# Kernel tuning notes

Measured on AMD Instinct MI355X. Metric: run time of the kernel, lower is better.

## Reference

```python
import jax, jax.numpy as jnp
import numpy as np

M = 64; N_SC = 32; SPS = 8; LENCP = 16; NUMOFDM = 256 // N_SC
BETA = 0.5; SPAN = 16; LENRRC = SPAN * SPS + 1  # 129
FC = 25e6; FS = 10e6 * SPS
CLIP = 1.2; SNR = 10.0; THRES = 8.0
LEN_T = NUMOFDM * (M + LENCP)              # 640
NUMSAMPLES = LEN_T * SPS + LENRRC * 2      # 5378
L1 = LEN_T * SPS + LENRRC - 1              # 5248 (post pulse-shaping length)


def make_rrc():
    # standard root-raised-cosine, unit energy
    t = np.arange(-SPAN * SPS // 2, SPAN * SPS // 2 + 1) / SPS
    h = np.zeros_like(t)
    eps = 1e-9
    t0 = np.abs(t) < eps
    ts = np.abs(np.abs(t) - 1.0 / (4 * BETA)) < eps
    reg = ~(t0 | ts)
    tr = t[reg]
    h[reg] = (np.sin(np.pi * tr * (1 - BETA)) + 4 * BETA * tr * np.cos(np.pi * tr * (1 + BETA))) / (
        np.pi * tr * (1 - (4 * BETA * tr) ** 2))
    h[t0] = 1 + BETA * (4 / np.pi - 1)
    h[ts] = (BETA / np.sqrt(2)) * ((1 + 2 / np.pi) * np.sin(np.pi / (4 * BETA)) +
                                   (1 - 2 / np.pi) * np.cos(np.pi / (4 * BETA)))
    h = h / np.sqrt(np.sum(h ** 2))
    return h.astype(np.float32)


def _conv_full(u, k):
    # torch F.conv1d(x, k.flip(), padding=K-1) == full convolution with k
    K = k.shape[0]
    return jax.lax.conv_general_dilated(
        u[:, None, :], k[::-1][None, None, :], (1,), [(K - 1, K - 1)],
        dimension_numbers=('NCH', 'OIH', 'NCH'))[:, 0, :]


def _pulse_filter(c, rrc):
    return _conv_full(c.real, rrc) + 1j * _conv_full(c.imag, rrc)


def _power_norm(z):
    m = jnp.mean(z, axis=1, keepdims=True)
    s = jnp.std(z, axis=1, ddof=1, keepdims=True)  # torch.std is unbiased
    return (z - m) / (s + 1e-8)


def _forward(x, W_enc, b_enc, W_dec, b_dec, rrc, awgn, startloc):
    B = x.shape[0]
    # --- encoder (linear proxy for ResNetTx) -> 512 reals ---
    z = x.reshape(B, -1) @ W_enc + b_enc
    z = _power_norm(z)
    c = z.reshape(B, 256, 2)
    c = (c[..., 0] + 1j * c[..., 1]).reshape(B, NUMOFDM, N_SC)  # complex64
    # --- DFT precoding ---
    c = jnp.fft.fftshift(jnp.fft.fft(c, axis=-1, norm='ortho'), axes=-1)
    # --- subcarrier mapping (contiguous block, mapping==1) ---
    loc = jnp.arange(startloc, startloc + N_SC)
    data_f = jnp.zeros((B, NUMOFDM, M), jnp.complex64).at[:, :, loc].set(c)
    data_t = jnp.fft.ifft(data_f, axis=-1, norm='ortho')
    data_t = jnp.concatenate([data_t[:, :, -LENCP:], data_t], axis=-1)  # CP
    data_t = data_t.reshape(B, LEN_T)
    # --- zero-stuffed upsampling + RRC pulse shaping ---
    over = jnp.zeros((B, LEN_T * SPS), jnp.complex64).at[:, ::SPS].set(data_t)
    xc = _pulse_filter(over, rrc)  # (B, L1)
    # --- carrier mixing ---
    n = jnp.arange(NUMSAMPLES, dtype=jnp.float32)
    cos_c = jnp.sqrt(2.0) * jnp.cos(2 * jnp.pi * FC * n / FS)
    sin_c = jnp.sqrt(2.0) * jnp.sin(2 * jnp.pi * FC * n / FS)
    data_x = xc.real * cos_c[:L1] - xc.imag * sin_c[:L1]
    # --- clipping ---
    thr = CLIP * jnp.sqrt(jnp.mean(jnp.square(data_x), axis=1, keepdims=True))
    over_amp = jax.nn.relu(jnp.abs(data_x) - thr)
    data_x = (1.0 - over_amp / (jnp.abs(data_x) + 1e-8)) * data_x
    # --- PAPR ---
    tstart = (LENRRC + 1) // 2
    p = jnp.square(data_x[:, tstart:tstart + LEN_T * SPS])
    PAPRdB = 10.0 * jnp.log10(jnp.max(p, axis=1) / jnp.mean(p, axis=1))
    PAPRloss = jnp.mean(jax.nn.relu(PAPRdB - THRES))
    # --- AWGN channel (no fading) ---
    data_r = data_x + awgn
    # --- downconversion + matched filter ---
    rc = data_r * cos_c[:L1] - 1j * (data_r * sin_c[:L1])
    filt = _pulse_filter(rc, rrc)  # (B, L1 + LENRRC - 1) = (B, 5376)
    y = filt[:, LENRRC - 1:filt.shape[1] - LENRRC:SPS]  # (B, LEN_T)
    y = y.reshape(B, NUMOFDM, M + LENCP)[:, :, LENCP:]
    y = jnp.fft.fft(y, axis=-1, norm='ortho')[:, :, loc]
    y = jnp.fft.ifft(jnp.fft.fftshift(y, axes=-1), axis=-1, norm='ortho')
    y = y.reshape(B, NUMOFDM * N_SC)
    y = jnp.stack([y.real, y.imag], axis=-1).reshape(B, 8, 8, 8)
    # --- decoder (linear proxy for ResNetRx) ---
    out = (y.reshape(B, 512) @ W_dec + b_dec).reshape(B, 3, 32, 32)
    return out, PAPRdB, PAPRloss


def setup_inputs() -> dict:
    key = jax.random.key(0)
    ks = jax.random.split(key, 4)
    B = 1024
    x = jax.random.normal(ks[0], (B, 3, 32, 32), jnp.float32)
    W_enc = jax.random.normal(ks[1], (3072, 512), jnp.float32) * 0.02
    b_enc = jnp.zeros((512,), jnp.float32)
    W_dec = jax.random.normal(ks[2], (512, 3072), jnp.float32) * 0.05
    b_dec = jnp.zeros((3072,), jnp.float32)
    rrc = jnp.asarray(make_rrc())
    noise_std = 10.0 ** (-SNR / 20.0)
    awgn = jax.random.normal(ks[3], (B, L1), jnp.float32) * noise_std
    return {"x": x, "W_enc": W_enc, "b_enc": b_enc, "W_dec": W_dec,
            "b_dec": b_dec, "rrc": rrc, "awgn": awgn, "startloc": 7}


def reference(x, W_enc, b_enc, W_dec, b_dec, rrc, awgn, startloc):
    return _forward(x, W_enc, b_enc, W_dec, b_dec, rrc, awgn, startloc)
```

## Files before the change

kernel.cpp:

```cpp
#include <hip/hip_runtime.h>
#include <hip/hip_bf16.h>
#include <math.h>

#define L1_     5248
#define LENRRC_ 129
#define TSTART_ 65
#define NWIN_   5120
#define SWZ(m) ((m) + ((m) >> 3))

typedef __attribute__((ext_vector_type(8))) short s16x8;
typedef __attribute__((ext_vector_type(4))) float f32x4;

__device__ inline ushort bf16_rne(float x) {
    unsigned xb = __float_as_uint(x);
    return (ushort)((xb + 0x7fffu + ((xb >> 16) & 1u)) >> 16);
}

__device__ inline float wave_sum(float v) {
    #pragma unroll
    for (int m = 32; m > 0; m >>= 1) v += __shfl_xor(v, m, 64);
    return v;
}
__device__ inline float wave_max(float v) {
    #pragma unroll
    for (int m = 32; m > 0; m >>= 1) v = fmaxf(v, __shfl_xor(v, m, 64));
    return v;
}

__device__ inline void gl_lds16(const void* g, void* l) {
    __builtin_amdgcn_global_load_lds(
        (const __attribute__((address_space(1))) unsigned int*)g,
        (__attribute__((address_space(3))) unsigned int*)l, 16, 0, 0);
}

__global__ __launch_bounds__(256) void pack_k(const float* __restrict__ x,
        const float* __restrict__ W1, const float* __restrict__ W2,
        const float* __restrict__ benc,
        ushort* __restrict__ xb, ushort* __restrict__ w1t, ushort* __restrict__ w2t,
        float* __restrict__ z)
{
    __shared__ ushort tile[64][70];
    const int blk = blockIdx.x, tid = threadIdx.x;
    if (blk < 3072) {
        int i = blk * 256 + tid;
        float4 v = ((const float4*)x)[i];
        ushort4 h;
        h.x = bf16_rne(v.x); h.y = bf16_rne(v.y);
        h.z = bf16_rne(v.z); h.w = bf16_rne(v.w);
        ((ushort4*)xb)[i] = h;
    } else if (blk < 3840) {
        const float* W; ushort* T; int K, N, n0, k0;
        if (blk < 3456) {
            int idx = blk - 3072;
            W = W1; T = w1t; K = 3072; N = 512;
            n0 = (idx & 7) * 64; k0 = (idx >> 3) * 64;
        } else {
            int idx = blk - 3456;
            W = W2; T = w2t; K = 512; N = 3072;
            n0 = (idx % 48) * 64; k0 = (idx / 48) * 64;
        }
        const int cr = tid >> 4, cc = (tid & 15) * 4;
        #pragma unroll
        for (int i = 0; i < 4; ++i) {
            int kk = i * 16 + cr;
            float4 v = *(const float4*)&W[(size_t)(k0 + kk) * N + n0 + cc];
            tile[kk][cc]     = bf16_rne(v.x);
            tile[kk][cc + 1] = bf16_rne(v.y);
            tile[kk][cc + 2] = bf16_rne(v.z);
            tile[kk][cc + 3] = bf16_rne(v.w);
        }
        __syncthreads();
        #pragma unroll
        for (int i = 0; i < 4; ++i) {
            int nn = i * 16 + cr;
            ushort4 h;
            h.x = tile[cc][nn]; h.y = tile[cc + 1][nn];
            h.z = tile[cc + 2][nn]; h.w = tile[cc + 3][nn];
            *(ushort4*)&T[(size_t)(n0 + nn) * K + k0 + cc] = h;
        }
    } else {
        int i = (blk - 3840) * 256 + tid;
        z[i] = benc[i & 511];
    }
}

__global__ __launch_bounds__(256) void gemm1_k(const ushort* __restrict__ Ab,
        const ushort* __restrict__ Bb, float* __restrict__ C, int M, int N, int K,
        int partial)
{
    __shared__ __attribute__((aligned(16))) ushort Asl[64 * 64];
    __shared__ __attribute__((aligned(16))) ushort Bsl[128 * 64];
    const int tid = threadIdx.x;
    const int lane = tid & 63, wave = tid >> 6;
    const int wm = (wave >> 1) * 32, wn = (wave & 1) * 64;
    const int m0 = blockIdx.y * 64, n0 = blockIdx.x * 128;
    const int kch = K / 8, kbeg = blockIdx.z * kch, kend = kbeg + kch;
    const int fm = lane & 15, q = lane >> 4;
    f32x4 acc[2][4] = {};

    int arow[2], akb[2], brow[4], bkb[4];
    #pragma unroll
    for (int j = 0; j < 2; ++j) {
        int c = ((wave * 2 + j) << 6) + lane;
        arow[j] = c >> 3; akb[j] = (c & 7) ^ (arow[j] & 7);
    }
    #pragma unroll
    for (int j = 0; j < 4; ++j) {
        int c = ((wave * 4 + j) << 6) + lane;
        brow[j] = c >> 3; bkb[j] = (c & 7) ^ (brow[j] & 7);
    }

    for (int kt = kbeg; kt < kend; kt += 64) {
        #pragma unroll
        for (int j = 0; j < 2; ++j)
            gl_lds16(&Ab[(size_t)(m0 + arow[j]) * K + kt + akb[j] * 8],
                     &Asl[(wave * 2 + j) << 9]);
        #pragma unroll
        for (int j = 0; j < 4; ++j)
            gl_lds16(&Bb[(size_t)(n0 + brow[j]) * K + kt + bkb[j] * 8],
                     &Bsl[(wave * 4 + j) << 9]);
        __syncthreads();
        #pragma unroll
        for (int ks = 0; ks < 2; ++ks) {
            s16x8 a[2], b[4];
            #pragma unroll
            for (int mf = 0; mf < 2; ++mf) {
                int r = wm + mf * 16 + fm;
                a[mf] = *(const s16x8*)&Asl[(r << 6) + ((((ks << 2) + q) ^ (r & 7)) << 3)];
            }
            #pragma unroll
            for (int nf = 0; nf < 4; ++nf) {
                int r = wn + nf * 16 + fm;
                b[nf] = *(const s16x8*)&Bsl[(r << 6) + ((((ks << 2) + q) ^ (r & 7)) << 3)];
            }
            #pragma unroll
            for (int mf = 0; mf < 2; ++mf)
                #pragma unroll
                for (int nf = 0; nf < 4; ++nf)
                    acc[mf][nf] = __builtin_amdgcn_mfma_f32_16x16x32_bf16(a[mf], b[nf], acc[mf][nf], 0, 0, 0);
        }
        __syncthreads();
    }

    if (partial) {
        float* Cs = C + (size_t)blockIdx.z * ((size_t)M * N);
        #pragma unroll
        for (int mf = 0; mf < 2; ++mf)
            #pragma unroll
            for (int nf = 0; nf < 4; ++nf)
                #pragma unroll
                for (int r = 0; r < 4; ++r) {
                    int m = m0 + wm + mf * 16 + q * 4 + r;
                    int n = n0 + wn + nf * 16 + fm;
                    Cs[(size_t)m * N + n] = acc[mf][nf][r];
                }
    } else {
        #pragma unroll
        for (int mf = 0; mf < 2; ++mf)
            #pragma unroll
            for (int nf = 0; nf < 4; ++nf)
                #pragma unroll
                for (int r = 0; r < 4; ++r) {
                    int m = m0 + wm + mf * 16 + q * 4 + r;
                    int n = n0 + wn + nf * 16 + fm;
                    atomicAdd(&C[(size_t)m * N + n], acc[mf][nf][r]);
                }
    }
}

__global__ __launch_bounds__(256) void gemm2_k(const ushort* __restrict__ Ab,
        const ushort* __restrict__ Bb, const float* __restrict__ bias,
        const float* __restrict__ papr, float* __restrict__ C,
        float* __restrict__ out_loss, int M, int N, int K)
{
    __shared__ __attribute__((aligned(16))) ushort Asl[64 * 64];
    __shared__ __attribute__((aligned(16))) ushort Bsl[64 * 64];
    __shared__ float red[4];
    const int tid = threadIdx.x;
    const int lane = tid & 63, wave = tid >> 6;
    const int wm = (wave >> 1) * 32, wn = (wave & 1) * 32;
    const int m0 = blockIdx.y * 64, n0 = blockIdx.x * 64;
    const int fm = lane & 15, q = lane >> 4;
    f32x4 acc[2][2] = {};

    int srow[2], skb[2];
    #pragma unroll
    for (int j = 0; j < 2; ++j) {
        int c = ((wave * 2 + j) << 6) + lane;
        srow[j] = c >> 3; skb[j] = (c & 7) ^ (srow[j] & 7);
    }

    for (int kt = 0; kt < K; kt += 64) {
        #pragma unroll
        for (int j = 0; j < 2; ++j) {
            gl_lds16(&Ab[(size_t)(m0 + srow[j]) * K + kt + skb[j] * 8],
                     &Asl[(wave * 2 + j) << 9]);
            gl_lds16(&Bb[(size_t)(n0 + srow[j]) * K + kt + skb[j] * 8],
                     &Bsl[(wave * 2 + j) << 9]);
        }
        __syncthreads();
        #pragma unroll
        for (int ks = 0; ks < 2; ++ks) {
            s16x8 a[2], b[2];
            #pragma unroll
            for (int mf = 0; mf < 2; ++mf) {
                int r = wm + mf * 16 + fm;
                a[mf] = *(const s16x8*)&Asl[(r << 6) + ((((ks << 2) + q) ^ (r & 7)) << 3)];
            }
            #pragma unroll
            for (int nf = 0; nf < 2; ++nf) {
                int r = wn + nf * 16 + fm;
                b[nf] = *(const s16x8*)&Bsl[(r << 6) + ((((ks << 2) + q) ^ (r & 7)) << 3)];
            }
            #pragma unroll
            for (int mf = 0; mf < 2; ++mf)
                #pragma unroll
                for (int nf = 0; nf < 2; ++nf)
                    acc[mf][nf] = __builtin_amdgcn_mfma_f32_16x16x32_bf16(a[mf], b[nf], acc[mf][nf], 0, 0, 0);
        }
        __syncthreads();
    }

    #pragma unroll
    for (int mf = 0; mf < 2; ++mf)
        #pragma unroll
        for (int nf = 0; nf < 2; ++nf)
            #pragma unroll
            for (int r = 0; r < 4; ++r) {
                int m = m0 + wm + mf * 16 + q * 4 + r;
                int n = n0 + wn + nf * 16 + fm;
                C[(size_t)m * N + n] = acc[mf][nf][r] + bias[n];
            }

    if (blockIdx.x == 0 && blockIdx.y == 0) {
        float s = 0.f;
        for (int i = tid; i < 1024; i += 256) { float v = papr[i] - 8.f; s += v > 0.f ? v : 0.f; }
        s = wave_sum(s);
        if (lane == 0) red[wave] = s;
        __syncthreads();
        if (tid == 0) *out_loss = (red[0] + red[1] + red[2] + red[3]) * (1.f / 1024.f);
    }
}

__global__ __launch_bounds__(512, 8) void mega_k(const float* __restrict__ z,
        const float* __restrict__ benc,
        const float* __restrict__ rrc, const float* __restrict__ awgn,
        const int* __restrict__ slocp, ushort* __restrict__ y5b,
        float* __restrict__ papr, float* __restrict__ out_papr, int nsp)
{
    __shared__ float  zl[512];
    __shared__ float2 frfi[8][32];
    __shared__ float2 trti[672];
    __shared__ float  hl[132];
    __shared__ float  csl[16], ssl[16];
    __shared__ float2 cs64[64];
    __shared__ float2 gcs[130];
    __shared__ float  dxr[SWZ(L1_ - 1) + 1];
    __shared__ float2 wrli[512];
    __shared__ float  red[8], red2[8];

    const int b = blockIdx.x, tid = threadIdx.x;
    const int lane = tid & 63, wv = tid >> 6;
    const int sloc = *slocp;

    if (tid < 64) {
        float ang = 0.09817477042468103f * (float)tid;
        float s, c; sincosf(ang, &s, &c);
        cs64[tid] = make_float2(c, s);
    }
    if (tid >= 64 && tid < 80) {
        int t = tid - 64;
        float ang = 1.9634954084936207f * (float)t;
        float s, c; sincosf(ang, &s, &c);
        csl[t] = 1.4142135623730951f * c; ssl[t] = 1.4142135623730951f * s;
    }
    if (tid >= 96 && tid < 128) {
        int t = tid - 96;
        int idx = (t < 16) ? t : (640 + t);
        trti[idx] = make_float2(0.f, 0.f);
    }
    if (tid < LENRRC_ + 256 && tid >= 256) hl[tid - 256] = rrc[tid - 256];
    if (tid >= 128 && tid < 131) hl[tid] = 0.f;

    float v0;
    if (nsp) {
        v0 = benc[tid];
        const float* zp = z + (size_t)b * 512;
        #pragma unroll
        for (int s = 0; s < 8; ++s)
            v0 += zp[(size_t)s * 524288 + tid];
    } else {
        v0 = z[(size_t)b * 512 + tid];
    }
    __syncthreads();

    if (tid < LENRRC_) {
        int neg = (16 - (tid & 15)) & 15;
        gcs[tid] = make_float2(hl[tid] * csl[neg], hl[tid] * ssl[neg]);
    }

    {
        float S = wave_sum(v0);
        float Q = wave_sum(v0 * v0);
        if (lane == 0) { red[wv] = S; red2[wv] = Q; }
    }
    __syncthreads();
    {
        float S = 0.f, Q = 0.f;
        #pragma unroll
        for (int w = 0; w < 8; ++w) { S += red[w]; Q += red2[w]; }
        float mean = S * (1.f / 512.f);
        float var = (Q - S * mean) * (1.f / 511.f);
        float inv = 1.f / (sqrtf(var) + 1e-8f);
        zl[tid] = (v0 - mean) * inv;
    }
    __syncthreads();

    if (tid < 256) {
        int s = tid >> 5, kk = tid & 31;
        int kk2 = (kk + 16) & 31;
        float sr = 0.f, si = 0.f;
        int t2 = 0;
        #pragma unroll 4
        for (int q = 0; q < 32; ++q) {
            float2 w = cs64[2 * t2];
            float2 c = *(const float2*)&zl[(s * 32 + q) * 2];
            sr += c.x * w.x + c.y * w.y;
            si += c.y * w.x - c.x * w.y;
            t2 = (t2 + kk2) & 31;
        }
        frfi[s][kk] = make_float2(sr * 0.1767766952966369f, si * 0.1767766952966369f);
    }
    __syncthreads();

    if (tid < 256) {
        int s = tid >> 5, n = tid & 31;
        float er = 0.f, ei = 0.f, or_ = 0.f, oi = 0.f;
        int t = (sloc * n) & 63;
        #pragma unroll 2
        for (int k = 0; k < 32; k += 2) {
            float2 w = cs64[t];
            float2 f = frfi[s][k];
            er += f.x * w.x - f.y * w.y;
            ei += f.y * w.x + f.x * w.y;
            t = (t + n) & 63;
            w = cs64[t];
            f = frfi[s][k + 1];
            or_ += f.x * w.x - f.y * w.y;
            oi  += f.y * w.x + f.x * w.y;
            t = (t + n) & 63;
        }
        float sgn = (sloc & 1) ? -1.f : 1.f;
        float dr0 = (er + or_) * 0.125f, di0 = (ei + oi) * 0.125f;
        float dr1 = sgn * (er - or_) * 0.125f, di1 = sgn * (ei - oi) * 0.125f;
        int base = s * 80;
        trti[base + 32 + n] = make_float2(dr0, di0);
        trti[base + 64 + n] = make_float2(dr1, di1);
        if (n >= 16) trti[base + n] = make_float2(dr1, di1);
    }
    __syncthreads();

    float ss = 0.f;
    for (int a = tid; a < 656; a += 512) {
        int cb = (a & 1) * 8;
        #pragma unroll
        for (int g = 0; g < 2; ++g) {
            float accr[4] = {}, acci[4] = {};
            #pragma unroll 4
            for (int d = 0; d < 16; ++d) {
                float2 tv = trti[16 + a - d];
                #pragma unroll
                for (int r = 0; r < 4; ++r) {
                    float h = hl[g * 4 + r + 8 * d];
                    accr[r] += tv.x * h; acci[r] += tv.y * h;
                }
            }
            if (g == 0) {
                float2 tv = trti[a];
                float h = hl[128];
                accr[0] += tv.x * h; acci[0] += tv.y * h;
            }
            #pragma unroll
            for (int r = 0; r < 4; ++r) {
                int rr = g * 4 + r;
                float v = accr[r] * csl[cb + rr] - acci[r] * ssl[cb + rr];
                dxr[SWZ(a * 8 + rr)] = v;
                ss += v * v;
            }
        }
    }
    ss = wave_sum(ss);
    if (lane == 0) red[wv] = ss;
    __syncthreads();
    float thr;
    {
        float S = 0.f;
        #pragma unroll
        for (int w = 0; w < 8; ++w) S += red[w];
        thr = 1.2f * sqrtf(S / (float)L1_);
    }
    __syncthreads();

    float pmax = 0.f, psum = 0.f;
    {
        const float4* ag = (const float4*)&awgn[(size_t)b * L1_];
        for (int ii = tid; ii < 1312; ii += 512) {
            float4 aw = ag[ii];
            int i = ii * 4;
            #pragma unroll
            for (int e = 0; e < 4; ++e) {
                int idx = i + e;
                float x = dxr[SWZ(idx)];
                float ax = fabsf(x);
                float over = fmaxf(ax - thr, 0.f);
                float y = (1.f - over / (ax + 1e-8f)) * x;
                if (idx >= TSTART_ && idx < TSTART_ + NWIN_) {
                    float p = y * y; psum += p; pmax = fmaxf(pmax, p);
                }
                float awv = (e == 0) ? aw.x : (e == 1) ? aw.y : (e == 2) ? aw.z : aw.w;
                dxr[SWZ(idx)] = y + awv;
            }
        }
    }
    psum = wave_sum(psum); pmax = wave_max(pmax);
    if (lane == 0) { red[wv] = psum; red2[wv] = pmax; }
    __syncthreads();
    if (tid == 0) {
        float sum = 0.f, mx = 0.f;
        #pragma unroll
        for (int w = 0; w < 8; ++w) { sum += red[w]; mx = fmaxf(mx, red2[w]); }
        float pdb = 10.f * log10f(mx / (sum / (float)NWIN_));
        papr[b] = pdb;
        out_papr[b] = pdb;
    }
    __syncthreads();

    {
        int s = tid >> 6, n = tid & 63;
        int T0 = s * 80 + n + 32;
        int base = 9 * T0;
        float ar = 0.f, ai = 0.f;
        int db = 0;
        #pragma unroll 4
        for (int e = 0; e < 16; ++e) {
            #pragma unroll
            for (int u = 0; u < 8; ++u) {
                int off = (u == 0) ? 0 : (u + 1);
                float2 g = gcs[db + u];
                float va = dxr[base - off];
                ar += va * g.x; ai += va * g.y;
            }
            base -= 9; db += 8;
        }
        {
            float2 g = gcs[128];
            float va = dxr[base];
            ar += va * g.x; ai += va * g.y;
        }
        bool odd = (n & 1);
        wrli[tid] = make_float2(odd ? -ar : ar, odd ? ai : -ai);
    }
    __syncthreads();

    {
        int h = tid >> 8, r = tid & 255;
        int s = r >> 5, n = r & 31;
        float2 d0 = wrli[s * 64 + n];
        float2 d1 = wrli[s * 64 + n + 32];
        float2 v = h ? make_float2(d0.x - d1.x, d0.y - d1.y)
                     : make_float2(d0.x + d1.x, d0.y + d1.y);
        trti[h * 256 + s * 32 + n] = v;
    }
    __syncthreads();

    if (tid < 256) {
        int s = tid >> 5, kk = tid & 31;
        int f = sloc + kk;
        const float2* dsel = &trti[((f & 1) ? 256 : 0) + s * 32];
        float vr = 0.f, vi = 0.f;
        int t = 0;
        #pragma unroll 4
        for (int n = 0; n < 32; ++n) {
            float2 w = cs64[t];
            float2 d = dsel[n];
            vr += d.x * w.x + d.y * w.y;
            vi += d.y * w.x - d.x * w.y;
            t = (t + f) & 63;
        }
        int ksh = (kk + 16) & 31;
        frfi[s][ksh] = make_float2(vr * 0.125f, vi * 0.125f);
    }
    __syncthreads();

    if (tid < 256) {
        int s = tid >> 5, q2 = tid & 31;
        float ur = 0.f, ui = 0.f;
        int t2 = 0;
        #pragma unroll 4
        for (int k = 0; k < 32; ++k) {
            float2 w = cs64[2 * t2];
            float2 f = frfi[s][k];
            ur += f.x * w.x - f.y * w.y;
            ui += f.y * w.x + f.x * w.y;
            t2 = (t2 + q2) & 31;
        }
        ur *= 0.1767766952966369f; ui *= 0.1767766952966369f;
        ushort2 hv; hv.x = bf16_rne(ur); hv.y = bf16_rne(ui);
        *(ushort2*)&y5b[(size_t)b * 512 + (s * 32 + q2) * 2] = hv;
    }
}

extern "C" void kernel_launch(void* const* d_in, const int* in_sizes, int n_in,
                              void* d_out, int out_size, void* d_ws, size_t ws_size,
                              hipStream_t stream) {
    const float* x    = (const float*)d_in[0];
    const float* Wenc = (const float*)d_in[1];
    const float* benc = (const float*)d_in[2];
    const float* Wdec = (const float*)d_in[3];
    const float* bdec = (const float*)d_in[4];
    const float* rrc  = (const float*)d_in[5];
    const float* awgn = (const float*)d_in[6];
    const int* sloc   = (const int*)d_in[7];
    float* out = (float*)d_out;

    char* wsb = (char*)d_ws;
    ushort* xb   = (ushort*)wsb;                     wsb += (size_t)1024 * 3072 * 2;
    ushort* w1t  = (ushort*)wsb;                     wsb += (size_t)512 * 3072 * 2;
    ushort* w2t  = (ushort*)wsb;                     wsb += (size_t)3072 * 512 * 2;
    ushort* y5b  = (ushort*)wsb;                     wsb += (size_t)1024 * 512 * 2;
    float*  papr = (float*)wsb;                      wsb += 1024 * 4;
    float*  zbuf = (float*)wsb;
    size_t head = (size_t)((char*)zbuf - (char*)d_ws);
    int partial = (ws_size >= head + (size_t)8 * 1024 * 512 * 4) ? 1 : 0;

    float* out_papr = out + (size_t)1024 * 3072;
    float* out_loss = out_papr + 1024;

    pack_k<<<partial ? 3840 : 5888, 256, 0, stream>>>(x, Wenc, Wdec, benc, xb, w1t, w2t, zbuf);
    gemm1_k<<<dim3(4, 16, 8), 256, 0, stream>>>(xb, w1t, zbuf, 1024, 512, 3072, partial);
    mega_k<<<1024, 512, 0, stream>>>(zbuf, benc, rrc, awgn, sloc, y5b, papr, out_papr,
                                     partial ? 8 : 0);
    gemm2_k<<<dim3(48, 16, 1), 256, 0, stream>>>(y5b, w2t, bdec, papr, out, out_loss, 1024, 3072, 512);
}
```

Measured before the change: 148.9 us.

## Double gemm1 split-K and spread mega_k DFT stages across all threads

The encoder GEMM's split-K factor goes from 8 to 16, giving more blocks in flight. The cost is a doubled partial-sum workspace, which mega_k must read back and reduce. Inside mega_k, each small DFT stage now splits its 32-term sums across thread pairs and combines them with a lane shuffle, so all 512 threads work instead of 256. The pulse-shaping convolution loop is split into finer tasks, and one butterfly stage plus its barrier and shared buffer are replaced by a cross-half-wave shuffle. This cuts idle threads and synchronisation, but adds shuffles and more global traffic for the partial sums.

```diff
diff --git a/kernel.cpp b/kernel.cpp
--- a/kernel.cpp
+++ b/kernel.cpp
@@ -86,7 +86,7 @@
 
 __global__ __launch_bounds__(256) void gemm1_k(const ushort* __restrict__ Ab,
         const ushort* __restrict__ Bb, float* __restrict__ C, int M, int N, int K,
-        int partial)
+        int partial, int nsp)
 {
     __shared__ __attribute__((aligned(16))) ushort Asl[64 * 64];
     __shared__ __attribute__((aligned(16))) ushort Bsl[128 * 64];
@@ -94,7 +94,7 @@
     const int lane = tid & 63, wave = tid >> 6;
     const int wm = (wave >> 1) * 32, wn = (wave & 1) * 64;
     const int m0 = blockIdx.y * 64, n0 = blockIdx.x * 128;
-    const int kch = K / 8, kbeg = blockIdx.z * kch, kend = kbeg + kch;
+    const int kch = K / nsp, kbeg = blockIdx.z * kch, kend = kbeg + kch;
     const int fm = lane & 15, q = lane >> 4;
     f32x4 acc[2][4] = {};
 
@@ -256,7 +256,6 @@
     __shared__ float2 cs64[64];
     __shared__ float2 gcs[130];
     __shared__ float  dxr[SWZ(L1_ - 1) + 1];
-    __shared__ float2 wrli[512];
     __shared__ float  red[8], red2[8];
 
     const int b = blockIdx.x, tid = threadIdx.x;
@@ -279,15 +278,13 @@
         int idx = (t < 16) ? t : (640 + t);
         trti[idx] = make_float2(0.f, 0.f);
     }
-    if (tid < LENRRC_ + 256 && tid >= 256) hl[tid - 256] = rrc[tid - 256];
-    if (tid >= 128 && tid < 131) hl[tid] = 0.f;
+    if (tid >= 256 && tid < 256 + LENRRC_) hl[tid - 256] = rrc[tid - 256];
 
     float v0;
     if (nsp) {
         v0 = benc[tid];
         const float* zp = z + (size_t)b * 512;
-        #pragma unroll
-        for (int s = 0; s < 8; ++s)
+        for (int s = 0; s < nsp; ++s)
             v0 += zp[(size_t)s * 524288 + tid];
     } else {
         v0 = z[(size_t)b * 512 + tid];
@@ -316,77 +313,86 @@
     }
     __syncthreads();
 
-    if (tid < 256) {
-        int s = tid >> 5, kk = tid & 31;
+    {
+        int out = tid >> 1, h = tid & 1;
+        int s = out >> 5, kk = out & 31;
         int kk2 = (kk + 16) & 31;
         float sr = 0.f, si = 0.f;
-        int t2 = 0;
+        int t2 = (16 * h * kk2) & 31;
+        int qb = s * 32 + 16 * h;
         #pragma unroll 4
-        for (int q = 0; q < 32; ++q) {
+        for (int q = 0; q < 16; ++q) {
             float2 w = cs64[2 * t2];
-            float2 c = *(const float2*)&zl[(s * 32 + q) * 2];
+            float2 c = *(const float2*)&zl[(qb + q) * 2];
             sr += c.x * w.x + c.y * w.y;
             si += c.y * w.x - c.x * w.y;
             t2 = (t2 + kk2) & 31;
         }
-        frfi[s][kk] = make_float2(sr * 0.1767766952966369f, si * 0.1767766952966369f);
-    }
-    __syncthreads();
-
-    if (tid < 256) {
-        int s = tid >> 5, n = tid & 31;
+        sr += __shfl_xor(sr, 1, 64);
+        si += __shfl_xor(si, 1, 64);
+        if (h == 0)
+            frfi[s][kk] = make_float2(sr * 0.1767766952966369f, si * 0.1767766952966369f);
+    }
+    __syncthreads();
+
+    {
+        int out = tid >> 1, h = tid & 1;
+        int s = out >> 5, n = out & 31;
         float er = 0.f, ei = 0.f, or_ = 0.f, oi = 0.f;
-        int t = (sloc * n) & 63;
+        int t = ((sloc + 16 * h) * n) & 63;
+        int kb = 16 * h;
         #pragma unroll 2
-        for (int k = 0; k < 32; k += 2) {
+        for (int k = 0; k < 16; k += 2) {
             float2 w = cs64[t];
-            float2 f = frfi[s][k];
+            float2 f = frfi[s][kb + k];
             er += f.x * w.x - f.y * w.y;
             ei += f.y * w.x + f.x * w.y;
             t = (t + n) & 63;
             w = cs64[t];
-            f = frfi[s][k + 1];
+            f = frfi[s][kb + k + 1];
             or_ += f.x * w.x - f.y * w.y;
             oi  += f.y * w.x + f.x * w.y;
             t = (t + n) & 63;
         }
-        float sgn = (sloc & 1) ? -1.f : 1.f;
-        float dr0 = (er + or_) * 0.125f, di0 = (ei + oi) * 0.125f;
-        float dr1 = sgn * (er - or_) * 0.125f, di1 = sgn * (ei - oi) * 0.125f;
-        int base = s * 80;
-        trti[base + 32 + n] = make_float2(dr0, di0);
-        trti[base + 64 + n] = make_float2(dr1, di1);
-        if (n >= 16) trti[base + n] = make_float2(dr1, di1);
+        er += __shfl_xor(er, 1, 64);  ei += __shfl_xor(ei, 1, 64);
+        or_ += __shfl_xor(or_, 1, 64); oi += __shfl_xor(oi, 1, 64);
+        if (h == 0) {
+            float sgn = (sloc & 1) ? -1.f : 1.f;
+            float dr0 = (er + or_) * 0.125f, di0 = (ei + oi) * 0.125f;
+            float dr1 = sgn * (er - or_) * 0.125f, di1 = sgn * (ei - oi) * 0.125f;
+            int base = s * 80;
+            trti[base + 32 + n] = make_float2(dr0, di0);
+            trti[base + 64 + n] = make_float2(dr1, di1);
+            if (n >= 16) trti[base + n] = make_float2(dr1, di1);
+        }
     }
     __syncthreads();
 
     float ss = 0.f;
-    for (int a = tid; a < 656; a += 512) {
+    for (int tsk = tid; tsk < 1312; tsk += 512) {
+        int a = tsk >> 1, g = tsk & 1;
+        float accr[4] = {}, acci[4] = {};
+        #pragma unroll 4
+        for (int d = 0; d < 16; ++d) {
+            float2 tv = trti[16 + a - d];
+            #pragma unroll
+            for (int r = 0; r < 4; ++r) {
+                float h = hl[g * 4 + r + 8 * d];
+                accr[r] += tv.x * h; acci[r] += tv.y * h;
+            }
+        }
+        if (g == 0) {
+            float2 tv = trti[a];
+            float h = hl[128];
+            accr[0] += tv.x * h; acci[0] += tv.y * h;
+        }
         int cb = (a & 1) * 8;
         #pragma unroll
-        for (int g = 0; g < 2; ++g) {
-            float accr[4] = {}, acci[4] = {};
-            #pragma unroll 4
-            for (int d = 0; d < 16; ++d) {
-                float2 tv = trti[16 + a - d];
-                #pragma unroll
-                for (int r = 0; r < 4; ++r) {
-                    float h = hl[g * 4 + r + 8 * d];
-                    accr[r] += tv.x * h; acci[r] += tv.y * h;
-                }
-            }
-            if (g == 0) {
-                float2 tv = trti[a];
-                float h = hl[128];
-                accr[0] += tv.x * h; acci[0] += tv.y * h;
-            }
-            #pragma unroll
-            for (int r = 0; r < 4; ++r) {
-                int rr = g * 4 + r;
-                float v = accr[r] * csl[cb + rr] - acci[r] * ssl[cb + rr];
-                dxr[SWZ(a * 8 + rr)] = v;
-                ss += v * v;
-            }
+        for (int r = 0; r < 4; ++r) {
+            int rr = g * 4 + r;
+            float v = accr[r] * csl[cb + rr] - acci[r] * ssl[cb + rr];
+            dxr[SWZ(a * 8 + rr)] = v;
+            ss += v * v;
         }
     }
     ss = wave_sum(ss);
@@ -436,7 +442,7 @@
     __syncthreads();
 
     {
-        int s = tid >> 6, n = tid & 63;
+        int s = wv, n = lane;
         int T0 = s * 80 + n + 32;
         int base = 9 * T0;
         float ar = 0.f, ai = 0.f;
@@ -458,55 +464,61 @@
             ar += va * g.x; ai += va * g.y;
         }
         bool odd = (n & 1);
-        wrli[tid] = make_float2(odd ? -ar : ar, odd ? ai : -ai);
-    }
-    __syncthreads();
-
-    {
-        int h = tid >> 8, r = tid & 255;
-        int s = r >> 5, n = r & 31;
-        float2 d0 = wrli[s * 64 + n];
-        float2 d1 = wrli[s * 64 + n + 32];
-        float2 v = h ? make_float2(d0.x - d1.x, d0.y - d1.y)
-                     : make_float2(d0.x + d1.x, d0.y + d1.y);
-        trti[h * 256 + s * 32 + n] = v;
-    }
-    __syncthreads();
-
-    if (tid < 256) {
-        int s = tid >> 5, kk = tid & 31;
+        float dx = odd ? -ar : ar;
+        float dy = odd ? ai : -ai;
+        float px = __shfl_xor(dx, 32, 64);
+        float py = __shfl_xor(dy, 32, 64);
+        float2 res = (n < 32) ? make_float2(dx + px, dy + py)
+                              : make_float2(px - dx, py - dy);
+        trti[((n >> 5) * 256) + s * 32 + (n & 31)] = res;
+    }
+    __syncthreads();
+
+    {
+        int out = tid >> 1, h = tid & 1;
+        int s = out >> 5, kk = out & 31;
         int f = sloc + kk;
-        const float2* dsel = &trti[((f & 1) ? 256 : 0) + s * 32];
+        const float2* dsel = &trti[((f & 1) ? 256 : 0) + s * 32 + 16 * h];
         float vr = 0.f, vi = 0.f;
-        int t = 0;
+        int t = (16 * h * f) & 63;
         #pragma unroll 4
-        for (int n = 0; n < 32; ++n) {
+        for (int n = 0; n < 16; ++n) {
             float2 w = cs64[t];
             float2 d = dsel[n];
             vr += d.x * w.x + d.y * w.y;
             vi += d.y * w.x - d.x * w.y;
             t = (t + f) & 63;
         }
-        int ksh = (kk + 16) & 31;
-        frfi[s][ksh] = make_float2(vr * 0.125f, vi * 0.125f);
-    }
-    __syncthreads();
-
-    if (tid < 256) {
-        int s = tid >> 5, q2 = tid & 31;
+        vr += __shfl_xor(vr, 1, 64);
+        vi += __shfl_xor(vi, 1, 64);
+        if (h == 0) {
+            int ksh = (kk + 16) & 31;
+            frfi[s][ksh] = make_float2(vr * 0.125f, vi * 0.125f);
+        }
+    }
+    __syncthreads();
+
+    {
+        int out = tid >> 1, h = tid & 1;
+        int s = out >> 5, q2 = out & 31;
         float ur = 0.f, ui = 0.f;
-        int t2 = 0;
+        int t2 = (16 * h * q2) & 31;
+        int kb = 16 * h;
         #pragma unroll 4
-        for (int k = 0; k < 32; ++k) {
+        for (int k = 0; k < 16; ++k) {
             float2 w = cs64[2 * t2];
-            float2 f = frfi[s][k];
+            float2 f = frfi[s][kb + k];
             ur += f.x * w.x - f.y * w.y;
             ui += f.y * w.x + f.x * w.y;
             t2 = (t2 + q2) & 31;
         }
-        ur *= 0.1767766952966369f; ui *= 0.1767766952966369f;
-        ushort2 hv; hv.x = bf16_rne(ur); hv.y = bf16_rne(ui);
-        *(ushort2*)&y5b[(size_t)b * 512 + (s * 32 + q2) * 2] = hv;
+        ur += __shfl_xor(ur, 1, 64);
+        ui += __shfl_xor(ui, 1, 64);
+        if (h == 0) {
+            ur *= 0.1767766952966369f; ui *= 0.1767766952966369f;
+            ushort2 hv; hv.x = bf16_rne(ur); hv.y = bf16_rne(ui);
+            *(ushort2*)&y5b[(size_t)b * 512 + (s * 32 + q2) * 2] = hv;
+        }
     }
 }
 
@@ -531,14 +543,16 @@
     float*  papr = (float*)wsb;                      wsb += 1024 * 4;
     float*  zbuf = (float*)wsb;
     size_t head = (size_t)((char*)zbuf - (char*)d_ws);
-    int partial = (ws_size >= head + (size_t)8 * 1024 * 512 * 4) ? 1 : 0;
+    const int SK = 16;
+    int partial = (ws_size >= head + (size_t)SK * 1024 * 512 * 4) ? 1 : 0;
 
     float* out_papr = out + (size_t)1024 * 3072;
     float* out_loss = out_papr + 1024;
 
     pack_k<<<partial ? 3840 : 5888, 256, 0, stream>>>(x, Wenc, Wdec, benc, xb, w1t, w2t, zbuf);
-    gemm1_k<<<dim3(4, 16, 8), 256, 0, stream>>>(xb, w1t, zbuf, 1024, 512, 3072, partial);
+    gemm1_k<<<dim3(4, 16, partial ? SK : 8), 256, 0, stream>>>(xb, w1t, zbuf, 1024, 512, 3072,
+                                                               partial, partial ? SK : 8);
     mega_k<<<1024, 512, 0, stream>>>(zbuf, benc, rrc, awgn, sloc, y5b, papr, out_papr,
-                                     partial ? 8 : 0);
+                                     partial ? SK : 0);
     gemm2_k<<<dim3(48, 16, 1), 256, 0, stream>>>(y5b, w2t, bdec, papr, out, out_loss, 1024, 3072, 512);
 }
```

After: 156.8 us. +5.3%, slower.

## Process two batch rows per block in mega kernel and shuffle final butterfly

Applied to the files above, without the earlier changes.

The per-sample signal-chain kernel now handles two batch rows per 512-thread block, halving the grid. Twiddle tables, filter taps and setup work are shared across both rows, and each LDS load of coefficients feeds two accumulators. The wrli staging buffer is removed in favour of a cross-half-wave shuffle butterfly, and gcs is read as float4. The cost is roughly double the shared memory per block and a lower launch-bounds occupancy hint, which together mean fewer resident blocks per CU to hide latency.

```diff
diff --git a/kernel.cpp b/kernel.cpp
--- a/kernel.cpp
+++ b/kernel.cpp
@@ -242,24 +242,24 @@
     }
 }
 
-__global__ __launch_bounds__(512, 8) void mega_k(const float* __restrict__ z,
+__global__ __launch_bounds__(512, 4) void mega_k(const float* __restrict__ z,
         const float* __restrict__ benc,
         const float* __restrict__ rrc, const float* __restrict__ awgn,
         const int* __restrict__ slocp, ushort* __restrict__ y5b,
         float* __restrict__ papr, float* __restrict__ out_papr, int nsp)
 {
-    __shared__ float  zl[512];
-    __shared__ float2 frfi[8][32];
-    __shared__ float2 trti[672];
+    __shared__ float  zl[2][512];
+    __shared__ float2 frfi[2][8][32];
+    __shared__ float2 trti[2][672];
     __shared__ float  hl[132];
     __shared__ float  csl[16], ssl[16];
     __shared__ float2 cs64[64];
-    __shared__ float2 gcs[130];
-    __shared__ float  dxr[SWZ(L1_ - 1) + 1];
-    __shared__ float2 wrli[512];
-    __shared__ float  red[8], red2[8];
-
-    const int b = blockIdx.x, tid = threadIdx.x;
+    __shared__ __attribute__((aligned(16))) float2 gcs[130];
+    __shared__ float  dxr[2][SWZ(L1_ - 1) + 1];
+    __shared__ float  red[2][8], red2[2][8];
+
+    const int b0 = blockIdx.x * 2, b1 = b0 + 1;
+    const int tid = threadIdx.x;
     const int lane = tid & 63, wv = tid >> 6;
     const int sloc = *slocp;
 
@@ -274,23 +274,25 @@
         float s, c; sincosf(ang, &s, &c);
         csl[t] = 1.4142135623730951f * c; ssl[t] = 1.4142135623730951f * s;
     }
-    if (tid >= 96 && tid < 128) {
-        int t = tid - 96;
+    if (tid >= 96 && tid < 160) {
+        int t = (tid - 96) & 31, row = (tid - 96) >> 5;
         int idx = (t < 16) ? t : (640 + t);
-        trti[idx] = make_float2(0.f, 0.f);
-    }
-    if (tid < LENRRC_ + 256 && tid >= 256) hl[tid - 256] = rrc[tid - 256];
-    if (tid >= 128 && tid < 131) hl[tid] = 0.f;
-
-    float v0;
+        trti[row][idx] = make_float2(0.f, 0.f);
+    }
+    if (tid >= 256 && tid < 256 + LENRRC_) hl[tid - 256] = rrc[tid - 256];
+
+    float va, vb;
     if (nsp) {
-        v0 = benc[tid];
-        const float* zp = z + (size_t)b * 512;
-        #pragma unroll
-        for (int s = 0; s < 8; ++s)
-            v0 += zp[(size_t)s * 524288 + tid];
+        va = benc[tid]; vb = va;
+        const float* zp0 = z + (size_t)b0 * 512;
+        const float* zp1 = z + (size_t)b1 * 512;
+        for (int s = 0; s < nsp; ++s) {
+            va += zp0[(size_t)s * 524288 + tid];
+            vb += zp1[(size_t)s * 524288 + tid];
+        }
     } else {
-        v0 = z[(size_t)b * 512 + tid];
+        va = z[(size_t)b0 * 512 + tid];
+        vb = z[(size_t)b1 * 512 + tid];
     }
     __syncthreads();
 
@@ -300,213 +302,273 @@
     }
 
     {
-        float S = wave_sum(v0);
-        float Q = wave_sum(v0 * v0);
-        if (lane == 0) { red[wv] = S; red2[wv] = Q; }
+        float S0 = wave_sum(va), Q0 = wave_sum(va * va);
+        float S1 = wave_sum(vb), Q1 = wave_sum(vb * vb);
+        if (lane == 0) { red[0][wv] = S0; red2[0][wv] = Q0; red[1][wv] = S1; red2[1][wv] = Q1; }
     }
     __syncthreads();
     {
-        float S = 0.f, Q = 0.f;
-        #pragma unroll
-        for (int w = 0; w < 8; ++w) { S += red[w]; Q += red2[w]; }
-        float mean = S * (1.f / 512.f);
-        float var = (Q - S * mean) * (1.f / 511.f);
-        float inv = 1.f / (sqrtf(var) + 1e-8f);
-        zl[tid] = (v0 - mean) * inv;
+        float S0 = 0.f, Q0 = 0.f, S1 = 0.f, Q1 = 0.f;
+        #pragma unroll
+        for (int w = 0; w < 8; ++w) {
+            S0 += red[0][w]; Q0 += red2[0][w];
+            S1 += red[1][w]; Q1 += red2[1][w];
+        }
+        float m0 = S0 * (1.f / 512.f), m1 = S1 * (1.f / 512.f);
+        float i0 = 1.f / (sqrtf((Q0 - S0 * m0) * (1.f / 511.f)) + 1e-8f);
+        float i1 = 1.f / (sqrtf((Q1 - S1 * m1) * (1.f / 511.f)) + 1e-8f);
+        zl[0][tid] = (va - m0) * i0;
+        zl[1][tid] = (vb - m1) * i1;
     }
     __syncthreads();
 
     if (tid < 256) {
         int s = tid >> 5, kk = tid & 31;
         int kk2 = (kk + 16) & 31;
-        float sr = 0.f, si = 0.f;
+        float sr0 = 0.f, si0 = 0.f, sr1 = 0.f, si1 = 0.f;
         int t2 = 0;
         #pragma unroll 4
         for (int q = 0; q < 32; ++q) {
             float2 w = cs64[2 * t2];
-            float2 c = *(const float2*)&zl[(s * 32 + q) * 2];
-            sr += c.x * w.x + c.y * w.y;
-            si += c.y * w.x - c.x * w.y;
+            float2 c0 = *(const float2*)&zl[0][(s * 32 + q) * 2];
+            float2 c1 = *(const float2*)&zl[1][(s * 32 + q) * 2];
+            sr0 += c0.x * w.x + c0.y * w.y;
+            si0 += c0.y * w.x - c0.x * w.y;
+            sr1 += c1.x * w.x + c1.y * w.y;
+            si1 += c1.y * w.x - c1.x * w.y;
             t2 = (t2 + kk2) & 31;
         }
-        frfi[s][kk] = make_float2(sr * 0.1767766952966369f, si * 0.1767766952966369f);
+        const float sc = 0.1767766952966369f;
+        frfi[0][s][kk] = make_float2(sr0 * sc, si0 * sc);
+        frfi[1][s][kk] = make_float2(sr1 * sc, si1 * sc);
     }
     __syncthreads();
 
     if (tid < 256) {
         int s = tid >> 5, n = tid & 31;
-        float er = 0.f, ei = 0.f, or_ = 0.f, oi = 0.f;
+        float er0 = 0.f, ei0 = 0.f, o_r0 = 0.f, o_i0 = 0.f;
+        float er1 = 0.f, ei1 = 0.f, o_r1 = 0.f, o_i1 = 0.f;
         int t = (sloc * n) & 63;
         #pragma unroll 2
         for (int k = 0; k < 32; k += 2) {
             float2 w = cs64[t];
-            float2 f = frfi[s][k];
-            er += f.x * w.x - f.y * w.y;
-            ei += f.y * w.x + f.x * w.y;
+            float2 f0 = frfi[0][s][k], f1 = frfi[1][s][k];
+            er0 += f0.x * w.x - f0.y * w.y;
+            ei0 += f0.y * w.x + f0.x * w.y;
+            er1 += f1.x * w.x - f1.y * w.y;
+            ei1 += f1.y * w.x + f1.x * w.y;
             t = (t + n) & 63;
             w = cs64[t];
-            f = frfi[s][k + 1];
-            or_ += f.x * w.x - f.y * w.y;
-            oi  += f.y * w.x + f.x * w.y;
+            f0 = frfi[0][s][k + 1]; f1 = frfi[1][s][k + 1];
+            o_r0 += f0.x * w.x - f0.y * w.y;
+            o_i0 += f0.y * w.x + f0.x * w.y;
+            o_r1 += f1.x * w.x - f1.y * w.y;
+            o_i1 += f1.y * w.x + f1.x * w.y;
             t = (t + n) & 63;
         }
         float sgn = (sloc & 1) ? -1.f : 1.f;
-        float dr0 = (er + or_) * 0.125f, di0 = (ei + oi) * 0.125f;
-        float dr1 = sgn * (er - or_) * 0.125f, di1 = sgn * (ei - oi) * 0.125f;
         int base = s * 80;
-        trti[base + 32 + n] = make_float2(dr0, di0);
-        trti[base + 64 + n] = make_float2(dr1, di1);
-        if (n >= 16) trti[base + n] = make_float2(dr1, di1);
-    }
-    __syncthreads();
-
-    float ss = 0.f;
-    for (int a = tid; a < 656; a += 512) {
+        {
+            float dr0 = (er0 + o_r0) * 0.125f, di0 = (ei0 + o_i0) * 0.125f;
+            float dr1 = sgn * (er0 - o_r0) * 0.125f, di1 = sgn * (ei0 - o_i0) * 0.125f;
+            trti[0][base + 32 + n] = make_float2(dr0, di0);
+            trti[0][base + 64 + n] = make_float2(dr1, di1);
+            if (n >= 16) trti[0][base + n] = make_float2(dr1, di1);
+        }
+        {
+            float dr0 = (er1 + o_r1) * 0.125f, di0 = (ei1 + o_i1) * 0.125f;
+            float dr1 = sgn * (er1 - o_r1) * 0.125f, di1 = sgn * (ei1 - o_i1) * 0.125f;
+            trti[1][base + 32 + n] = make_float2(dr0, di0);
+            trti[1][base + 64 + n] = make_float2(dr1, di1);
+            if (n >= 16) trti[1][base + n] = make_float2(dr1, di1);
+        }
+    }
+    __syncthreads();
+
+    float ss0 = 0.f, ss1 = 0.f;
+    for (int tsk = tid; tsk < 1312; tsk += 512) {
+        int a = tsk >> 1, g = tsk & 1;
+        float ar0[4] = {}, ai0[4] = {}, ar1[4] = {}, ai1[4] = {};
+        #pragma unroll 4
+        for (int d = 0; d < 16; ++d) {
+            float2 t0 = trti[0][16 + a - d];
+            float2 t1 = trti[1][16 + a - d];
+            #pragma unroll
+            for (int r = 0; r < 4; ++r) {
+                float h = hl[g * 4 + r + 8 * d];
+                ar0[r] += t0.x * h; ai0[r] += t0.y * h;
+                ar1[r] += t1.x * h; ai1[r] += t1.y * h;
+            }
+        }
+        if (g == 0) {
+            float2 t0 = trti[0][a], t1 = trti[1][a];
+            float h = hl[128];
+            ar0[0] += t0.x * h; ai0[0] += t0.y * h;
+            ar1[0] += t1.x * h; ai1[0] += t1.y * h;
+        }
         int cb = (a & 1) * 8;
         #pragma unroll
-        for (int g = 0; g < 2; ++g) {
-            float accr[4] = {}, acci[4] = {};
-            #pragma unroll 4
-            for (int d = 0; d < 16; ++d) {
-                float2 tv = trti[16 + a - d];
-                #pragma unroll
-                for (int r = 0; r < 4; ++r) {
-                    float h = hl[g * 4 + r + 8 * d];
-                    accr[r] += tv.x * h; acci[r] += tv.y * h;
-                }
-            }
-            if (g == 0) {
-                float2 tv = trti[a];
-                float h = hl[128];
-                accr[0] += tv.x * h; acci[0] += tv.y * h;
-            }
-            #pragma unroll
-            for (int r = 0; r < 4; ++r) {
-                int rr = g * 4 + r;
-                float v = accr[r] * csl[cb + rr] - acci[r] * ssl[cb + rr];
-                dxr[SWZ(a * 8 + rr)] = v;
-                ss += v * v;
-            }
-        }
-    }
-    ss = wave_sum(ss);
-    if (lane == 0) red[wv] = ss;
-    __syncthreads();
-    float thr;
+        for (int r = 0; r < 4; ++r) {
+            int rr = g * 4 + r;
+            float cv = csl[cb + rr], sv = ssl[cb + rr];
+            float v0 = ar0[r] * cv - ai0[r] * sv;
+            float v1 = ar1[r] * cv - ai1[r] * sv;
+            dxr[0][SWZ(a * 8 + rr)] = v0;
+            dxr[1][SWZ(a * 8 + rr)] = v1;
+            ss0 += v0 * v0; ss1 += v1 * v1;
+        }
+    }
+    ss0 = wave_sum(ss0); ss1 = wave_sum(ss1);
+    if (lane == 0) { red[0][wv] = ss0; red[1][wv] = ss1; }
+    __syncthreads();
+    float thr0, thr1;
     {
-        float S = 0.f;
-        #pragma unroll
-        for (int w = 0; w < 8; ++w) S += red[w];
-        thr = 1.2f * sqrtf(S / (float)L1_);
-    }
-    __syncthreads();
-
-    float pmax = 0.f, psum = 0.f;
+        float S0 = 0.f, S1 = 0.f;
+        #pragma unroll
+        for (int w = 0; w < 8; ++w) { S0 += red[0][w]; S1 += red[1][w]; }
+        thr0 = 1.2f * sqrtf(S0 / (float)L1_);
+        thr1 = 1.2f * sqrtf(S1 / (float)L1_);
+    }
+    __syncthreads();
+
+    float pm0 = 0.f, ps0 = 0.f, pm1 = 0.f, ps1 = 0.f;
     {
-        const float4* ag = (const float4*)&awgn[(size_t)b * L1_];
+        const float4* ag0 = (const float4*)&awgn[(size_t)b0 * L1_];
+        const float4* ag1 = (const float4*)&awgn[(size_t)b1 * L1_];
         for (int ii = tid; ii < 1312; ii += 512) {
-            float4 aw = ag[ii];
+            float4 a0 = ag0[ii], a1 = ag1[ii];
             int i = ii * 4;
             #pragma unroll
             for (int e = 0; e < 4; ++e) {
                 int idx = i + e;
-                float x = dxr[SWZ(idx)];
-                float ax = fabsf(x);
-                float over = fmaxf(ax - thr, 0.f);
-                float y = (1.f - over / (ax + 1e-8f)) * x;
-                if (idx >= TSTART_ && idx < TSTART_ + NWIN_) {
-                    float p = y * y; psum += p; pmax = fmaxf(pmax, p);
+                bool win = (idx >= TSTART_ && idx < TSTART_ + NWIN_);
+                float aw0 = (e == 0) ? a0.x : (e == 1) ? a0.y : (e == 2) ? a0.z : a0.w;
+                float aw1 = (e == 0) ? a1.x : (e == 1) ? a1.y : (e == 2) ? a1.z : a1.w;
+                {
+                    float x = dxr[0][SWZ(idx)];
+                    float ax = fabsf(x);
+                    float over = fmaxf(ax - thr0, 0.f);
+                    float y = (1.f - over / (ax + 1e-8f)) * x;
+                    if (win) { float p = y * y; ps0 += p; pm0 = fmaxf(pm0, p); }
+                    dxr[0][SWZ(idx)] = y + aw0;
                 }
-                float awv = (e == 0) ? aw.x : (e == 1) ? aw.y : (e == 2) ? aw.z : aw.w;
-                dxr[SWZ(idx)] = y + awv;
-            }
-        }
-    }
-    psum = wave_sum(psum); pmax = wave_max(pmax);
-    if (lane == 0) { red[wv] = psum; red2[wv] = pmax; }
+                {
+                    float x = dxr[1][SWZ(idx)];
+                    float ax = fabsf(x);
+                    float over = fmaxf(ax - thr1, 0.f);
+                    float y = (1.f - over / (ax + 1e-8f)) * x;
+                    if (win) { float p = y * y; ps1 += p; pm1 = fmaxf(pm1, p); }
+                    dxr[1][SWZ(idx)] = y + aw1;
+                }
+            }
+        }
+    }
+    ps0 = wave_sum(ps0); pm0 = wave_max(pm0);
+    ps1 = wave_sum(ps1); pm1 = wave_max(pm1);
+    if (lane == 0) { red[0][wv] = ps0; red2[0][wv] = pm0; red[1][wv] = ps1; red2[1][wv] = pm1; }
     __syncthreads();
     if (tid == 0) {
-        float sum = 0.f, mx = 0.f;
-        #pragma unroll
-        for (int w = 0; w < 8; ++w) { sum += red[w]; mx = fmaxf(mx, red2[w]); }
-        float pdb = 10.f * log10f(mx / (sum / (float)NWIN_));
-        papr[b] = pdb;
-        out_papr[b] = pdb;
+        float s0 = 0.f, m0 = 0.f, s1 = 0.f, m1 = 0.f;
+        #pragma unroll
+        for (int w = 0; w < 8; ++w) {
+            s0 += red[0][w]; m0 = fmaxf(m0, red2[0][w]);
+            s1 += red[1][w]; m1 = fmaxf(m1, red2[1][w]);
+        }
+        float p0 = 10.f * log10f(m0 / (s0 / (float)NWIN_));
+        float p1 = 10.f * log10f(m1 / (s1 / (float)NWIN_));
+        papr[b0] = p0; out_papr[b0] = p0;
+        papr[b1] = p1; out_papr[b1] = p1;
     }
     __syncthreads();
 
     {
-        int s = tid >> 6, n = tid & 63;
+        int s = wv, n = lane;
         int T0 = s * 80 + n + 32;
         int base = 9 * T0;
-        float ar = 0.f, ai = 0.f;
+        float ar0 = 0.f, ai0 = 0.f, ar1 = 0.f, ai1 = 0.f;
         int db = 0;
         #pragma unroll 4
         for (int e = 0; e < 16; ++e) {
+            float4 g01 = *(const float4*)&gcs[db];
+            float4 g23 = *(const float4*)&gcs[db + 2];
+            float4 g45 = *(const float4*)&gcs[db + 4];
+            float4 g67 = *(const float4*)&gcs[db + 6];
+            float gx[8] = { g01.x, g01.z, g23.x, g23.z, g45.x, g45.z, g67.x, g67.z };
+            float gy[8] = { g01.y, g01.w, g23.y, g23.w, g45.y, g45.w, g67.y, g67.w };
             #pragma unroll
             for (int u = 0; u < 8; ++u) {
                 int off = (u == 0) ? 0 : (u + 1);
-                float2 g = gcs[db + u];
-                float va = dxr[base - off];
-                ar += va * g.x; ai += va * g.y;
+                float v0 = dxr[0][base - off];
+                float v1 = dxr[1][base - off];
+                ar0 += v0 * gx[u]; ai0 += v0 * gy[u];
+                ar1 += v1 * gx[u]; ai1 += v1 * gy[u];
             }
             base -= 9; db += 8;
         }
         {
             float2 g = gcs[128];
-            float va = dxr[base];
-            ar += va * g.x; ai += va * g.y;
+            float v0 = dxr[0][base], v1 = dxr[1][base];
+            ar0 += v0 * g.x; ai0 += v0 * g.y;
+            ar1 += v1 * g.x; ai1 += v1 * g.y;
         }
         bool odd = (n & 1);
-        wrli[tid] = make_float2(odd ? -ar : ar, odd ? ai : -ai);
-    }
-    __syncthreads();
-
-    {
-        int h = tid >> 8, r = tid & 255;
-        int s = r >> 5, n = r & 31;
-        float2 d0 = wrli[s * 64 + n];
-        float2 d1 = wrli[s * 64 + n + 32];
-        float2 v = h ? make_float2(d0.x - d1.x, d0.y - d1.y)
-                     : make_float2(d0.x + d1.x, d0.y + d1.y);
-        trti[h * 256 + s * 32 + n] = v;
+        float dx0 = odd ? -ar0 : ar0, dy0 = odd ? ai0 : -ai0;
+        float dx1 = odd ? -ar1 : ar1, dy1 = odd ? ai1 : -ai1;
+        float px0 = __shfl_xor(dx0, 32, 64), py0 = __shfl_xor(dy0, 32, 64);
+        float px1 = __shfl_xor(dx1, 32, 64), py1 = __shfl_xor(dy1, 32, 64);
+        float2 r0 = (n < 32) ? make_float2(dx0 + px0, dy0 + py0)
+                             : make_float2(px0 - dx0, py0 - dy0);
+        float2 r1 = (n < 32) ? make_float2(dx1 + px1, dy1 + py1)
+                             : make_float2(px1 - dx1, py1 - dy1);
+        int di = ((n >> 5) * 256) + s * 32 + (n & 31);
+        trti[0][di] = r0;
+        trti[1][di] = r1;
     }
     __syncthreads();
 
     if (tid < 256) {
         int s = tid >> 5, kk = tid & 31;
         int f = sloc + kk;
-        const float2* dsel = &trti[((f & 1) ? 256 : 0) + s * 32];
-        float vr = 0.f, vi = 0.f;
+        int doff = ((f & 1) ? 256 : 0) + s * 32;
+        const float2* d0 = &trti[0][doff];
+        const float2* d1 = &trti[1][doff];
+        float vr0 = 0.f, vi0 = 0.f, vr1 = 0.f, vi1 = 0.f;
         int t = 0;
         #pragma unroll 4
         for (int n = 0; n < 32; ++n) {
             float2 w = cs64[t];
-            float2 d = dsel[n];
-            vr += d.x * w.x + d.y * w.y;
-            vi += d.y * w.x - d.x * w.y;
+            float2 e0 = d0[n], e1 = d1[n];
+            vr0 += e0.x * w.x + e0.y * w.y;
+            vi0 += e0.y * w.x - e0.x * w.y;
+            vr1 += e1.x * w.x + e1.y * w.y;
+            vi1 += e1.y * w.x - e1.x * w.y;
             t = (t + f) & 63;
         }
         int ksh = (kk + 16) & 31;
-        frfi[s][ksh] = make_float2(vr * 0.125f, vi * 0.125f);
+        frfi[0][s][ksh] = make_float2(vr0 * 0.125f, vi0 * 0.125f);
+        frfi[1][s][ksh] = make_float2(vr1 * 0.125f, vi1 * 0.125f);
     }
     __syncthreads();
 
     if (tid < 256) {
         int s = tid >> 5, q2 = tid & 31;
-        float ur = 0.f, ui = 0.f;
+        float ur0 = 0.f, ui0 = 0.f, ur1 = 0.f, ui1 = 0.f;
         int t2 = 0;
         #pragma unroll 4
         for (int k = 0; k < 32; ++k) {
             float2 w = cs64[2 * t2];
-            float2 f = frfi[s][k];
-            ur += f.x * w.x - f.y * w.y;
-            ui += f.y * w.x + f.x * w.y;
+            float2 f0 = frfi[0][s][k], f1 = frfi[1][s][k];
+            ur0 += f0.x * w.x - f0.y * w.y;
+            ui0 += f0.y * w.x + f0.x * w.y;
+            ur1 += f1.x * w.x - f1.y * w.y;
+            ui1 += f1.y * w.x + f1.x * w.y;
             t2 = (t2 + q2) & 31;
         }
-        ur *= 0.1767766952966369f; ui *= 0.1767766952966369f;
-        ushort2 hv; hv.x = bf16_rne(ur); hv.y = bf16_rne(ui);
-        *(ushort2*)&y5b[(size_t)b * 512 + (s * 32 + q2) * 2] = hv;
+        const float sc = 0.1767766952966369f;
+        ushort2 h0; h0.x = bf16_rne(ur0 * sc); h0.y = bf16_rne(ui0 * sc);
+        ushort2 h1; h1.x = bf16_rne(ur1 * sc); h1.y = bf16_rne(ui1 * sc);
+        *(ushort2*)&y5b[(size_t)b0 * 512 + (s * 32 + q2) * 2] = h0;
+        *(ushort2*)&y5b[(size_t)b1 * 512 + (s * 32 + q2) * 2] = h1;
     }
 }
 
@@ -538,7 +600,7 @@
 
     pack_k<<<partial ? 3840 : 5888, 256, 0, stream>>>(x, Wenc, Wdec, benc, xb, w1t, w2t, zbuf);
     gemm1_k<<<dim3(4, 16, 8), 256, 0, stream>>>(xb, w1t, zbuf, 1024, 512, 3072, partial);
-    mega_k<<<1024, 512, 0, stream>>>(zbuf, benc, rrc, awgn, sloc, y5b, papr, out_papr,
-                                     partial ? 8 : 0);
+    mega_k<<<512, 512, 0, stream>>>(zbuf, benc, rrc, awgn, sloc, y5b, papr, out_papr,
+                                    partial ? 8 : 0);
     gemm2_k<<<dim3(48, 16, 1), 256, 0, stream>>>(y5b, w2t, bdec, papr, out, out_loss, 1024, 3072, 512);
 }
```

Result: no change. 147.7 us (-0.8%).
